# Kernel tuning notes

Hardware: AMD Instinct MI355X
Metric: run time of the kernel (lower is better)

Reference implementation:

```python
import jax, jax.numpy as jnp
import numpy as np

N = 1_000_000
C = 128
B = 16  # number of instances (batch segments)
EPS = 1e-5


def setup_inputs() -> dict:
    key = jax.random.key(0)
    k1, k2 = jax.random.split(key)
    x = jax.random.normal(k1, (N, C), dtype=jnp.float32)
    batch_idx = jnp.sort(jax.random.randint(k2, (N,), 0, B, dtype=jnp.int32))
    weight = jnp.ones((1, C), dtype=jnp.float32)
    bias = jnp.zeros((1, C), dtype=jnp.float32)
    return {"x": x, "batch_idx": batch_idx, "weight": weight, "bias": bias}


def reference(x, batch_idx, weight, bias):
    # per-instance counts [B, 1]
    cnt = jax.ops.segment_sum(jnp.ones((x.shape[0], 1), x.dtype), batch_idx,
                              num_segments=B)
    cnt = jnp.maximum(cnt, 1.0)
    # segment mean [B, C]
    mean = jax.ops.segment_sum(x, batch_idx, num_segments=B) / cnt
    centered = x - mean[batch_idx]               # broadcast-add of -mean
    # segment mean of squared centered features -> per-instance variance [B, C]
    var = jax.ops.segment_sum(centered * centered, batch_idx, num_segments=B) / cnt
    instd = 1.0 / jnp.sqrt(var + EPS)            # [B, C]
    # broadcast-multiply, then affine
    return centered * instd[batch_idx] * weight + bias
```

## Files before the change

### kernel.cpp

```cpp
#include <hip/hip_runtime.h>

#define CC 128
#define BSEG 16
#define EPSV 1e-5f
#define ROWS_PER_BLOCK 512
#define NORM_GRID 2048

typedef float v4f __attribute__((ext_vector_type(4)));

__device__ __forceinline__ int lower_bound_dev(const int* __restrict__ a, int n, int v)
{
    int lo = 0, hi = n;
    while (lo < hi) {
        const int mid = (lo + hi) >> 1;
        if (a[mid] < v) lo = mid + 1; else hi = mid;
    }
    return lo;
}

__global__ __launch_bounds__(256) void ms_stats(const float* __restrict__ x,
                                                const int* __restrict__ bidx,
                                                int n,
                                                float* __restrict__ sum,
                                                float* __restrict__ sumsq)
{
    const int r0 = blockIdx.x * ROWS_PER_BLOCK;
    if (r0 >= n) return;
    const int rend = min(r0 + ROWS_PER_BLOCK, n);
    const int tq = threadIdx.x & 31;
    const int tr = threadIdx.x >> 5;

    const int seg_first = bidx[r0];
    const int seg_last  = bidx[rend - 1];

    v4f s = {0.f, 0.f, 0.f, 0.f};
    v4f q = {0.f, 0.f, 0.f, 0.f};

    if (seg_first == seg_last) {
        int r = r0 + tr;
        for (; r + 8 < rend; r += 16) {
            const v4f a = *reinterpret_cast<const v4f*>(x + (size_t)r * CC + tq * 4);
            const v4f b = *reinterpret_cast<const v4f*>(x + (size_t)(r + 8) * CC + tq * 4);
            s += a; q += a * a;
            s += b; q += b * b;
        }
        if (r < rend) {
            const v4f a = *reinterpret_cast<const v4f*>(x + (size_t)r * CC + tq * 4);
            s += a; q += a * a;
        }
        __shared__ float red[8][8][32];
        red[tr][0][tq] = s.x; red[tr][1][tq] = s.y; red[tr][2][tq] = s.z; red[tr][3][tq] = s.w;
        red[tr][4][tq] = q.x; red[tr][5][tq] = q.y; red[tr][6][tq] = q.z; red[tr][7][tq] = q.w;
        __syncthreads();
        const int j = threadIdx.x >> 5;
        float acc = 0.f;
        #pragma unroll
        for (int k = 0; k < 8; ++k) acc += red[k][j][tq];
        const int ch = tq * 4 + (j & 3);
        atomicAdd(((j < 4) ? sum : sumsq) + seg_first * CC + ch, acc);
    } else {
        int cur = -1;
        for (int r = r0 + tr; r < rend; r += 8) {
            const int seg = bidx[r];
            if (seg != cur) {
                if (cur >= 0) {
                    float* sd = sum   + cur * CC + tq * 4;
                    float* qd = sumsq + cur * CC + tq * 4;
                    atomicAdd(sd + 0, s.x); atomicAdd(sd + 1, s.y);
                    atomicAdd(sd + 2, s.z); atomicAdd(sd + 3, s.w);
                    atomicAdd(qd + 0, q.x); atomicAdd(qd + 1, q.y);
                    atomicAdd(qd + 2, q.z); atomicAdd(qd + 3, q.w);
                    s = (v4f){0.f, 0.f, 0.f, 0.f};
                    q = (v4f){0.f, 0.f, 0.f, 0.f};
                }
                cur = seg;
            }
            const v4f a = *reinterpret_cast<const v4f*>(x + (size_t)r * CC + tq * 4);
            s += a; q += a * a;
        }
        if (cur >= 0) {
            float* sd = sum   + cur * CC + tq * 4;
            float* qd = sumsq + cur * CC + tq * 4;
            atomicAdd(sd + 0, s.x); atomicAdd(sd + 1, s.y);
            atomicAdd(sd + 2, s.z); atomicAdd(sd + 3, s.w);
            atomicAdd(qd + 0, q.x); atomicAdd(qd + 1, q.y);
            atomicAdd(qd + 2, q.z); atomicAdd(qd + 3, q.w);
        }
    }
}

__global__ __launch_bounds__(256) void ms_norm(const float* __restrict__ x,
                                               const int* __restrict__ bidx,
                                               const float* __restrict__ sum,
                                               const float* __restrict__ sumsq,
                                               const float* __restrict__ w,
                                               const float* __restrict__ bias,
                                               float* __restrict__ out,
                                               int n)
{
    __shared__ int sbs[BSEG + 1];
    __shared__ v4f s_scale[BSEG * 32];
    __shared__ v4f s_shift[BSEG * 32];

    if (threadIdx.x <= BSEG)
        sbs[threadIdx.x] = lower_bound_dev(bidx, n, (int)threadIdx.x);
    __syncthreads();

    for (int i = threadIdx.x; i < BSEG * CC; i += 256) {
        const int b = i >> 7;
        const int c = i & (CC - 1);
        const float nn   = fmaxf((float)(sbs[b + 1] - sbs[b]), 1.0f);
        const float mean = sum[i] / nn;
        const float var  = fmaxf(sumsq[i] / nn - mean * mean, 0.0f);
        const float sc   = rsqrtf(var + EPSV) * w[c];
        reinterpret_cast<float*>(s_scale)[i] = sc;
        reinterpret_cast<float*>(s_shift)[i] = fmaf(-mean, sc, bias[c]);
    }
    __syncthreads();

    int rb[BSEG - 1];
    #pragma unroll
    for (int i = 0; i < BSEG - 1; ++i) rb[i] = sbs[i + 1];

    const int total = n * 16;
    const int T     = (int)(gridDim.x * blockDim.x);

    for (int p = total - 1 - (int)(blockIdx.x * blockDim.x + threadIdx.x);
         p >= 0; p -= T) {
        const int r = p >> 4;
        int seg = 0;
        #pragma unroll
        for (int i = 0; i < BSEG - 1; ++i) seg += (r >= rb[i]);

        const v4f a = reinterpret_cast<const v4f*>(x)[2 * (size_t)p];
        const v4f b = reinterpret_cast<const v4f*>(x)[2 * (size_t)p + 1];
        const int ti = seg * 32 + (p & 15) * 2;
        const v4f sca = s_scale[ti], scb = s_scale[ti + 1];
        const v4f sha = s_shift[ti], shb = s_shift[ti + 1];
        v4f oa, ob;
        oa.x = fmaf(a.x, sca.x, sha.x); oa.y = fmaf(a.y, sca.y, sha.y);
        oa.z = fmaf(a.z, sca.z, sha.z); oa.w = fmaf(a.w, sca.w, sha.w);
        ob.x = fmaf(b.x, scb.x, shb.x); ob.y = fmaf(b.y, scb.y, shb.y);
        ob.z = fmaf(b.z, scb.z, shb.z); ob.w = fmaf(b.w, scb.w, shb.w);
        __builtin_nontemporal_store(oa, reinterpret_cast<v4f*>(out) + 2 * (size_t)p);
        __builtin_nontemporal_store(ob, reinterpret_cast<v4f*>(out) + 2 * (size_t)p + 1);
    }
}

extern "C" void kernel_launch(void* const* d_in, const int* in_sizes, int n_in,
                              void* d_out, int out_size, void* d_ws, size_t ws_size,
                              hipStream_t stream)
{
    const float* x    = (const float*)d_in[0];
    const int*   bidx = (const int*)d_in[1];
    const float* w    = (const float*)d_in[2];
    const float* bias = (const float*)d_in[3];
    float* out = (float*)d_out;
    const int n = in_sizes[1];

    float* ws    = (float*)d_ws;
    float* sum   = ws;
    float* sumsq = ws + BSEG * CC;

    (void)hipMemsetAsync(d_ws, 0, (size_t)(2 * BSEG * CC) * sizeof(float), stream);

    const int g1 = (n + ROWS_PER_BLOCK - 1) / ROWS_PER_BLOCK;
    ms_stats<<<g1, 256, 0, stream>>>(x, bidx, n, sum, sumsq);
    ms_norm<<<NORM_GRID, 256, 0, stream>>>(x, bidx, sum, sumsq, w, bias, out, n);
}
```

Measured before the change: 322.4 us.

## Tile normalize pass by block with uniform-segment fast path and unrolled loads

The normalize kernel now gives each block contiguous tiles of 2048 row-pairs instead of a grid-stride walk over individual pairs. When a tile lies within one segment, scale and shift are loaded from shared memory once and eight iterations are fully unrolled, which removes the per-element segment search and LDS reads and raises memory-level parallelism. Tiles that cross a segment boundary fall back to the per-element path. The kernel is memory-bound, so the gain depends on whether more loads in flight improve bandwidth use.

```diff
diff --git a/kernel.cpp b/kernel.cpp
--- a/kernel.cpp
+++ b/kernel.cpp
@@ -5,6 +5,7 @@
 #define EPSV 1e-5f
 #define ROWS_PER_BLOCK 512
 #define NORM_GRID 2048
+#define TILE_PAIRS 2048
 
 typedef float v4f __attribute__((ext_vector_type(4)));
 
@@ -122,28 +123,71 @@
     #pragma unroll
     for (int i = 0; i < BSEG - 1; ++i) rb[i] = sbs[i + 1];
 
-    const int total = n * 16;
-    const int T     = (int)(gridDim.x * blockDim.x);
-
-    for (int p = total - 1 - (int)(blockIdx.x * blockDim.x + threadIdx.x);
-         p >= 0; p -= T) {
-        const int r = p >> 4;
-        int seg = 0;
-        #pragma unroll
-        for (int i = 0; i < BSEG - 1; ++i) seg += (r >= rb[i]);
-
-        const v4f a = reinterpret_cast<const v4f*>(x)[2 * (size_t)p];
-        const v4f b = reinterpret_cast<const v4f*>(x)[2 * (size_t)p + 1];
-        const int ti = seg * 32 + (p & 15) * 2;
-        const v4f sca = s_scale[ti], scb = s_scale[ti + 1];
-        const v4f sha = s_shift[ti], shb = s_shift[ti + 1];
-        v4f oa, ob;
-        oa.x = fmaf(a.x, sca.x, sha.x); oa.y = fmaf(a.y, sca.y, sha.y);
-        oa.z = fmaf(a.z, sca.z, sha.z); oa.w = fmaf(a.w, sca.w, sha.w);
-        ob.x = fmaf(b.x, scb.x, shb.x); ob.y = fmaf(b.y, scb.y, shb.y);
-        ob.z = fmaf(b.z, scb.z, shb.z); ob.w = fmaf(b.w, scb.w, shb.w);
-        __builtin_nontemporal_store(oa, reinterpret_cast<v4f*>(out) + 2 * (size_t)p);
-        __builtin_nontemporal_store(ob, reinterpret_cast<v4f*>(out) + 2 * (size_t)p + 1);
+    const int total  = n * 16;
+    const int ntiles = (total + TILE_PAIRS - 1) / TILE_PAIRS;
+    const int tid    = (int)threadIdx.x;
+    const v4f* __restrict__ x4 = reinterpret_cast<const v4f*>(x);
+    v4f* __restrict__ out4     = reinterpret_cast<v4f*>(out);
+    const int tloc = 2 * (tid & 15);
+
+    for (int t = ntiles - 1 - (int)blockIdx.x; t >= 0; t -= (int)gridDim.x) {
+        const int pbase = t * TILE_PAIRS;
+        const int pend  = min(pbase + TILE_PAIRS, total);
+        const int sA = bidx[pbase >> 4];
+        const int sB = bidx[(pend - 1) >> 4];
+
+        if (sA == sB) {
+            const int ti = sA * 32 + tloc;
+            const v4f sca = s_scale[ti], scb = s_scale[ti + 1];
+            const v4f sha = s_shift[ti], shb = s_shift[ti + 1];
+
+            if (pend == pbase + TILE_PAIRS) {
+                const size_t f0 = 2 * (size_t)(pbase + tid);
+                #pragma unroll
+                for (int j = 0; j < 8; ++j) {
+                    const size_t fi = f0 + (size_t)j * 512;
+                    const v4f a = x4[fi], b = x4[fi + 1];
+                    v4f oa, ob;
+                    oa.x = fmaf(a.x, sca.x, sha.x); oa.y = fmaf(a.y, sca.y, sha.y);
+                    oa.z = fmaf(a.z, sca.z, sha.z); oa.w = fmaf(a.w, sca.w, sha.w);
+                    ob.x = fmaf(b.x, scb.x, shb.x); ob.y = fmaf(b.y, scb.y, shb.y);
+                    ob.z = fmaf(b.z, scb.z, shb.z); ob.w = fmaf(b.w, scb.w, shb.w);
+                    __builtin_nontemporal_store(oa, out4 + fi);
+                    __builtin_nontemporal_store(ob, out4 + fi + 1);
+                }
+            } else {
+                for (int p = pbase + tid; p < pend; p += 256) {
+                    const size_t fi = 2 * (size_t)p;
+                    const v4f a = x4[fi], b = x4[fi + 1];
+                    v4f oa, ob;
+                    oa.x = fmaf(a.x, sca.x, sha.x); oa.y = fmaf(a.y, sca.y, sha.y);
+                    oa.z = fmaf(a.z, sca.z, sha.z); oa.w = fmaf(a.w, sca.w, sha.w);
+                    ob.x = fmaf(b.x, scb.x, shb.x); ob.y = fmaf(b.y, scb.y, shb.y);
+                    ob.z = fmaf(b.z, scb.z, shb.z); ob.w = fmaf(b.w, scb.w, shb.w);
+                    __builtin_nontemporal_store(oa, out4 + fi);
+                    __builtin_nontemporal_store(ob, out4 + fi + 1);
+                }
+            }
+        } else {
+            for (int p = pbase + tid; p < pend; p += 256) {
+                const int r = p >> 4;
+                int seg = 0;
+                #pragma unroll
+                for (int i = 0; i < BSEG - 1; ++i) seg += (r >= rb[i]);
+                const int ti = seg * 32 + tloc;
+                const v4f sca = s_scale[ti], scb = s_scale[ti + 1];
+                const v4f sha = s_shift[ti], shb = s_shift[ti + 1];
+                const size_t fi = 2 * (size_t)p;
+                const v4f a = x4[fi], b = x4[fi + 1];
+                v4f oa, ob;
+                oa.x = fmaf(a.x, sca.x, sha.x); oa.y = fmaf(a.y, sca.y, sha.y);
+                oa.z = fmaf(a.z, sca.z, sha.z); oa.w = fmaf(a.w, sca.w, sha.w);
+                ob.x = fmaf(b.x, scb.x, shb.x); ob.y = fmaf(b.y, scb.y, shb.y);
+                ob.z = fmaf(b.z, scb.z, shb.z); ob.w = fmaf(b.w, scb.w, shb.w);
+                __builtin_nontemporal_store(oa, out4 + fi);
+                __builtin_nontemporal_store(ob, out4 + fi + 1);
+            }
+        }
     }
 }
 
```

After: 467.4 us. 1.45x slower.
